# Kernel optimization log

Hardware: AMD Instinct MI355X
Metric: run time of the kernel (lower is better)

Reference implementation:

```python
import jax, jax.numpy as jnp
import numpy as np

N_NODES = 50000
N_EDGES = 800000
IN_DIM = 128
HID = 32
HEADS = 4
OUT_DIM = 128
NEG_SLOPE = 0.2


def setup_inputs() -> dict:
    key = jax.random.key(0)
    ks = jax.random.split(key, 10)
    s = lambda fan_in: 1.0 / np.sqrt(fan_in)
    return {
        "x": jax.random.normal(ks[0], (N_NODES, IN_DIM), dtype=jnp.float32),
        "edge_index": jax.random.randint(ks[1], (2, N_EDGES), 0, N_NODES, dtype=jnp.int64),
        # encoder GATConv: in=IN_DIM, out=HID, heads=HEADS (concat)
        "W1": jax.random.normal(ks[2], (IN_DIM, HEADS * HID), dtype=jnp.float32) * s(IN_DIM),
        "att_src1": jax.random.normal(ks[3], (HEADS, HID), dtype=jnp.float32) * s(HID),
        "att_dst1": jax.random.normal(ks[4], (HEADS, HID), dtype=jnp.float32) * s(HID),
        "b1": jnp.zeros((HEADS * HID,), dtype=jnp.float32),
        # decoder GATConv: in=HEADS*HID, out=OUT_DIM, heads=1
        "W2": jax.random.normal(ks[5], (HEADS * HID, OUT_DIM), dtype=jnp.float32) * s(HEADS * HID),
        "att_src2": jax.random.normal(ks[6], (1, OUT_DIM), dtype=jnp.float32) * s(OUT_DIM),
        "att_dst2": jax.random.normal(ks[7], (1, OUT_DIM), dtype=jnp.float32) * s(OUT_DIM),
        "b2": jnp.zeros((OUT_DIM,), dtype=jnp.float32),
    }


def _gat_conv(x, src, dst, W, att_src, att_dst, bias, heads, out_ch):
    """PyG-style GATConv (v1), eval mode (dropout off), self-loops already in src/dst."""
    n = x.shape[0]
    h = (x @ W).reshape(n, heads, out_ch)                 # [N,H,C]
    a_src = jnp.einsum("nhc,hc->nh", h, att_src)          # [N,H]
    a_dst = jnp.einsum("nhc,hc->nh", h, att_dst)          # [N,H]
    e = jax.nn.leaky_relu(a_src[src] + a_dst[dst], NEG_SLOPE)  # [E,H]
    # segment softmax over destination neighborhoods
    e_max = jax.ops.segment_max(e, dst, num_segments=n)   # [N,H]
    e_exp = jnp.exp(e - e_max[dst])
    denom = jax.ops.segment_sum(e_exp, dst, num_segments=n)
    alpha = e_exp / (denom[dst] + 1e-16)                  # [E,H]
    msg = h[src] * alpha[:, :, None]                      # [E,H,C]
    out = jax.ops.segment_sum(msg, dst, num_segments=n)   # [N,H,C]
    return out.reshape(n, heads * out_ch) + bias


def reference(x, edge_index, W1, att_src1, att_dst1, b1, W2, att_src2, att_dst2, b2):
    n = x.shape[0]
    loops = jnp.arange(n, dtype=edge_index.dtype)
    src = jnp.concatenate([edge_index[0], loops])
    dst = jnp.concatenate([edge_index[1], loops])
    z = jax.nn.relu(_gat_conv(x, src, dst, W1, att_src1, att_dst1, b1, HEADS, HID))
    x_hat = jax.nn.relu(_gat_conv(z, src, dst, W2, att_src2, att_dst2, b2, 1, OUT_DIM))
    return x_hat
```

## Files before the change

kernel.cpp:

```cpp
#include <hip/hip_runtime.h>
#include <hip/hip_bf16.h>
#include <cstddef>

#define N_NODES 50000
#define N_EDGES_RAW 800000
#define E_TOT (N_EDGES_RAW + N_NODES)
#define DIM 128
#define NEG_SLOPE 0.2f

#define NBUCK 196
#define CHUNK 4096
#define NBLK_E ((E_TOT + CHUNK - 1) / CHUNK)
#define CONV_BLKS 3125
#define GB 782

typedef __attribute__((ext_vector_type(8))) short bf16x8;
typedef __attribute__((ext_vector_type(4))) float f32x4;

__device__ __forceinline__ ushort f2bf(float f) {
  unsigned u = __float_as_uint(f);
  return (ushort)((u + 0x7FFFu + ((u >> 16) & 1u)) >> 16);
}
__device__ __forceinline__ float bf2f_lo(uint u) {
  return __uint_as_float(u << 16);
}
__device__ __forceinline__ float bf2f_hi(uint u) {
  return __uint_as_float(u & 0xFFFF0000u);
}

__device__ __forceinline__ void get_edge(const int* __restrict__ ei, int is64,
                                         int e, int& s, int& d) {
  if (e >= N_EDGES_RAW) { s = e - N_EDGES_RAW; d = s; return; }
  if (is64) {
    s = ei[2 * (size_t)e];
    d = ei[2 * ((size_t)N_EDGES_RAW + (size_t)e)];
  } else {
    s = ei[e];
    d = ei[N_EDGES_RAW + e];
  }
}

__device__ __forceinline__ int detect_inline(const int* __restrict__ ei,
                                             int* sflag) {
  const int t = threadIdx.x;
  if (t < 64) {
    int hi = ei[2 * t + 1];
    unsigned long long b = __ballot(hi != 0);
    if (t == 0) *sflag = (b == 0ULL) ? 1 : 0;
  }
  __syncthreads();
  return *sflag;
}

__device__ __forceinline__ void prep_one(const float* __restrict__ w,
                                         const float* __restrict__ atts,
                                         const float* __restrict__ attd,
                                         ushort* __restrict__ wtx,
                                         int H, int idx) {
  const int c = idx >> 7, k = idx & 127;
  const int C = 128 / H;
  float v;
  if (c < 128) {
    v = w[k * 128 + c];
  } else if (c < 128 + H) {
    const int hd = c - 128;
    float s = 0.f;
    for (int j = 0; j < C; ++j) s += w[k * 128 + hd * C + j] * atts[hd * C + j];
    v = s;
  } else if (c < 128 + 2 * H) {
    const int hd = c - 128 - H;
    float s = 0.f;
    for (int j = 0; j < C; ++j) s += w[k * 128 + hd * C + j] * attd[hd * C + j];
    v = s;
  } else {
    v = 0.f;
  }
  wtx[idx] = f2bf(v);
}

__global__ __launch_bounds__(256) void mega_setup(
    const int* __restrict__ ei, int* __restrict__ hist_mat,
    unsigned* __restrict__ pairs,
    const float* __restrict__ W1, const float* __restrict__ as1,
    const float* __restrict__ ad1,
    const float* __restrict__ W2, const float* __restrict__ as2,
    const float* __restrict__ ad2,
    const float* __restrict__ x, ushort* __restrict__ x_bf,
    ushort* __restrict__ wtx1, ushort* __restrict__ wtx2,
    float* __restrict__ w_as2, float* __restrict__ w_ad2) {
  const int b = blockIdx.x, t = threadIdx.x;
  if (b < 72) {
    prep_one(W1, as1, ad1, wtx1, 4, b * 256 + t);
  } else if (b < 136) {
    const int idx = (b - 72) * 256 + t;
    const int c = idx >> 7, k = idx & 127;
    wtx2[idx] = f2bf(W2[k * 128 + c]);
  } else if (b == 136) {
    if (t < 128) {
      float s2 = 0.f, d2 = 0.f;
      for (int c = 0; c < 128; ++c) {
        float w = W2[t * 128 + c];
        s2 += w * as2[c];
        d2 += w * ad2[c];
      }
      w_as2[t] = s2;
      w_ad2[t] = d2;
    }
  } else if (b < 137 + CONV_BLKS) {
    const int base = (b - 137) * 2048 + t * 8;
    float4 v0 = *(const float4*)(x + base);
    float4 v1 = *(const float4*)(x + base + 4);
    ushort u[8];
    u[0] = f2bf(v0.x); u[1] = f2bf(v0.y); u[2] = f2bf(v0.z); u[3] = f2bf(v0.w);
    u[4] = f2bf(v1.x); u[5] = f2bf(v1.y); u[6] = f2bf(v1.z); u[7] = f2bf(v1.w);
    *(uint4*)(x_bf + base) = *(const uint4*)u;
  } else {
    __shared__ int hist[NBUCK];
    __shared__ int sflag;
    const int cb = b - 137 - CONV_BLKS;
    if (t < NBUCK) hist[t] = 0;
    const int is64 = detect_inline(ei, &sflag);
    __syncthreads();
    const int e0 = cb * CHUNK;
#pragma unroll
    for (int i = 0; i < CHUNK / 256; ++i) {
      int e = e0 + i * 256 + t;
      if (e < E_TOT) {
        int s, d;
        get_edge(ei, is64, e, s, d);
        pairs[e] = (unsigned)s | ((unsigned)d << 16);
        atomicAdd(&hist[d >> 8], 1);
      }
    }
    __syncthreads();
    if (t < NBUCK) hist_mat[cb * NBUCK + t] = hist[t];
  }
}

__global__ __launch_bounds__(256) void bucket_scatter(
    const unsigned* __restrict__ pairs, const int* __restrict__ hist_mat,
    unsigned* __restrict__ tmp, int* __restrict__ bstart_g) {
  __shared__ int wtot[4];
  __shared__ int sbase[NBUCK];
  __shared__ int shist[NBUCK];
  const int b = blockIdx.x, t = threadIdx.x, lane = t & 63, wid = t >> 6;
  int tot = 0, pre = 0;
  if (t < NBUCK) {
    for (int bb = 0; bb < NBLK_E; ++bb) {
      int v = hist_mat[bb * NBUCK + t];
      pre += (bb < b) ? v : 0;
      tot += v;
    }
    shist[t] = 0;
  }
  int sc = tot;
#pragma unroll
  for (int m = 1; m < 64; m <<= 1) {
    int o = __shfl_up(sc, m, 64);
    if (lane >= m) sc += o;
  }
  if (lane == 63) wtot[wid] = sc;
  __syncthreads();
  int off = 0;
  for (int w = 0; w < wid; ++w) off += wtot[w];
  const int excl = off + sc - tot;
  if (t < NBUCK) sbase[t] = excl + pre;
  if (b == 0) {
    if (t < NBUCK) bstart_g[t] = excl;
    if (t == 255) bstart_g[NBUCK] = off + sc;
  }
  __syncthreads();
  const int e0 = b * CHUNK;
  unsigned pr_[CHUNK / 256];
  int rk[CHUNK / 256];
#pragma unroll
  for (int i = 0; i < CHUNK / 256; ++i) {
    int e = e0 + i * 256 + t;
    if (e < E_TOT) {
      unsigned pr = pairs[e];
      pr_[i] = pr;
      rk[i] = atomicAdd(&shist[pr >> 24], 1);
    }
  }
#pragma unroll
  for (int i = 0; i < CHUNK / 256; ++i) {
    int e = e0 + i * 256 + t;
    if (e < E_TOT) tmp[sbase[pr_[i] >> 24] + rk[i]] = pr_[i];
  }
}

__device__ __forceinline__ void bucket_sort_body(int b,
                                                 const unsigned* __restrict__ tmp,
                                                 const int* __restrict__ bstart,
                                                 unsigned* __restrict__ csr2,
                                                 int* __restrict__ rp,
                                                 int* __restrict__ deg) {
  __shared__ int cnt[256];
  __shared__ int cur[256];
  __shared__ int wtot2[4];
  const int t = threadIdx.x, lane = t & 63, wid = t >> 6;
  const int p0 = bstart[b], p1 = bstart[b + 1];
  cnt[t] = 0;
  __syncthreads();
  for (int j = p0 + t; j < p1; j += 256) {
    unsigned pr = tmp[j];
    atomicAdd(&cnt[(pr >> 16) & 255u], 1);
  }
  __syncthreads();
  int v = cnt[t];
  int sc = v;
#pragma unroll
  for (int m = 1; m < 64; m <<= 1) {
    int o = __shfl_up(sc, m, 64);
    if (lane >= m) sc += o;
  }
  if (lane == 63) wtot2[wid] = sc;
  __syncthreads();
  int off = 0;
  for (int w = 0; w < wid; ++w) off += wtot2[w];
  const int excl = off + sc - v;
  const int node = b * 256 + t;
  if (node < N_NODES) {
    deg[node] = v;
    rp[node] = p0 + excl;
  }
  cur[t] = excl;
  __syncthreads();
  for (int j = p0 + t; j < p1; j += 256) {
    unsigned pr = tmp[j];
    int ld = (int)((pr >> 16) & 255u);
    int r = atomicAdd(&cur[ld], 1);
    csr2[p0 + r] = pr;
  }
}

__device__ __forceinline__ void gemm_att_body4(int blk,
                                               const ushort* __restrict__ in_bf,
                                               const ushort* __restrict__ wtx,
                                               ushort* __restrict__ h_bf,
                                               float* __restrict__ a_src,
                                               float* __restrict__ a_dst) {
  const int wid = threadIdx.x >> 6;
  const int lane = threadIdx.x & 63;
  const int tile = blk * 4 + wid;
  if (tile >= N_NODES / 16) return;
  const int row0 = tile * 16;
  const int rA = lane & 15;
  const int g = lane >> 4;

  f32x4 acc[9];
#pragma unroll
  for (int ct = 0; ct < 9; ++ct) acc[ct] = (f32x4){0.f, 0.f, 0.f, 0.f};

#pragma unroll
  for (int ks = 0; ks < 4; ++ks) {
    const int k0 = ks * 32 + g * 8;
    bf16x8 af = *(const bf16x8*)(in_bf + (size_t)(row0 + rA) * DIM + k0);
#pragma unroll
    for (int ct = 0; ct < 9; ++ct) {
      bf16x8 bf = *(const bf16x8*)(wtx + (size_t)(ct * 16 + rA) * 128 + k0);
      acc[ct] = __builtin_amdgcn_mfma_f32_16x16x32_bf16(af, bf, acc[ct], 0, 0, 0);
    }
  }

#pragma unroll
  for (int ct = 0; ct < 8; ++ct) {
#pragma unroll
    for (int r = 0; r < 4; ++r) {
      const int row = row0 + g * 4 + r;
      h_bf[(size_t)row * DIM + ct * 16 + rA] = f2bf(acc[ct][r]);
    }
  }
  if (rA < 8) {
#pragma unroll
    for (int r = 0; r < 4; ++r) {
      const int row = row0 + g * 4 + r;
      if (rA < 4)
        a_src[(size_t)row * 4 + rA] = acc[8][r];
      else
        a_dst[(size_t)row * 4 + (rA - 4)] = acc[8][r];
    }
  }
}

__global__ __launch_bounds__(256) void gemm4_sort(
    const ushort* __restrict__ x_bf, const ushort* __restrict__ wtx1,
    ushort* __restrict__ h_bf, float* __restrict__ a_src,
    float* __restrict__ a_dst, const unsigned* __restrict__ tmp,
    const int* __restrict__ bstart, unsigned* __restrict__ csr2,
    int* __restrict__ rp, int* __restrict__ deg) {
  if (blockIdx.x < GB)
    gemm_att_body4(blockIdx.x, x_bf, wtx1, h_bf, a_src, a_dst);
  else
    bucket_sort_body(blockIdx.x - GB, tmp, bstart, csr2, rp, deg);
}

__global__ __launch_bounds__(256) void node_agg_l1(
    const int* __restrict__ rp, const int* __restrict__ deg,
    const unsigned* __restrict__ csr2, const ushort* __restrict__ h_bf,
    const float* __restrict__ a_srcv, const float* __restrict__ a_dstv,
    const float* __restrict__ bias, const float* __restrict__ w_as2,
    const float* __restrict__ w_ad2, ushort* __restrict__ z_bf,
    float* __restrict__ a_src2, float* __restrict__ a_dst2) {
  __shared__ float p_lds[4][4][68];
  __shared__ int s_lds[4][64];
  const int wid = threadIdx.x >> 6;
  const int lane = threadIdx.x & 63;
  const int node = blockIdx.x * 4 + wid;
  const int head = lane >> 4;
  const int beg = rp[node];
  const int dg = deg[node];

  float ad[4];
#pragma unroll
  for (int h = 0; h < 4; ++h) ad[h] = a_dstv[(size_t)node * 4 + h];

  float sden = 0.f, ax = 0.f, ay = 0.f;

  for (int c0 = 0; c0 < dg; c0 += 64) {
    const int cnt = min(64, dg - c0);
    if (lane < cnt) {
      int s = (int)(csr2[beg + c0 + lane] & 0xFFFFu);
      s_lds[wid][lane] = s;
      float4 as4 = ((const float4*)a_srcv)[s];
      float vv[4] = {as4.x, as4.y, as4.z, as4.w};
#pragma unroll
      for (int h = 0; h < 4; ++h) {
        float v = vv[h] + ad[h];
        v = v > 0.f ? v : NEG_SLOPE * v;
        v = fminf(fmaxf(v, -60.f), 80.f);
        p_lds[wid][h][lane] = __expf(v);
      }
    }
    int j = 0;
    for (; j + 8 <= cnt; j += 8) {
#pragma unroll
      for (int u = 0; u < 8; ++u) {
        int s = s_lds[wid][j + u];
        float p = p_lds[wid][head][j + u];
        uint hv = *(const uint*)(h_bf + (size_t)s * DIM + 2 * lane);
        ax += p * bf2f_lo(hv);
        ay += p * bf2f_hi(hv);
        sden += p;
      }
    }
    for (; j < cnt; ++j) {
      int s = s_lds[wid][j];
      float p = p_lds[wid][head][j];
      uint hv = *(const uint*)(h_bf + (size_t)s * DIM + 2 * lane);
      ax += p * bf2f_lo(hv);
      ay += p * bf2f_hi(hv);
      sden += p;
    }
  }

  const float inv = 1.f / sden;
  float2 bv = ((const float2*)bias)[lane];
  float ox = fmaxf(ax * inv + bv.x, 0.f);
  float oy = fmaxf(ay * inv + bv.y, 0.f);
  uint u = (uint)f2bf(ox) | ((uint)f2bf(oy) << 16);
  ((uint*)(z_bf + (size_t)node * DIM))[lane] = u;

  float2 ws = ((const float2*)w_as2)[lane];
  float2 wd = ((const float2*)w_ad2)[lane];
  float ps = ox * ws.x + oy * ws.y;
  float pd = ox * wd.x + oy * wd.y;
#pragma unroll
  for (int m = 1; m < 64; m <<= 1) {
    ps += __shfl_xor(ps, m);
    pd += __shfl_xor(pd, m);
  }
  if (lane == 0) {
    a_src2[node] = ps;
    a_dst2[node] = pd;
  }
}

__global__ __launch_bounds__(256) void node_agg_l2(
    const int* __restrict__ rp, const int* __restrict__ deg,
    const unsigned* __restrict__ csr2, const ushort* __restrict__ z_bf,
    const float* __restrict__ a_src2, const float* __restrict__ a_dst2,
    const ushort* __restrict__ wtx2, const float* __restrict__ bias,
    float* __restrict__ outp) {
  __shared__ float p_lds[4][68];
  __shared__ int s_lds[4][64];
  __shared__ ushort u_lds[16][136];
  const int wid = threadIdx.x >> 6;
  const int lane = threadIdx.x & 63;
  const int node = blockIdx.x * 4 + wid;
  const int beg = rp[node];
  const int dg = deg[node];
  const float ad = a_dst2[node];

  float sden = 0.f, ax = 0.f, ay = 0.f;

  for (int c0 = 0; c0 < dg; c0 += 64) {
    const int cnt = min(64, dg - c0);
    if (lane < cnt) {
      int s = (int)(csr2[beg + c0 + lane] & 0xFFFFu);
      s_lds[wid][lane] = s;
      float v = a_src2[s] + ad;
      v = v > 0.f ? v : NEG_SLOPE * v;
      v = fminf(fmaxf(v, -60.f), 80.f);
      p_lds[wid][lane] = __expf(v);
    }
    int j = 0;
    for (; j + 8 <= cnt; j += 8) {
#pragma unroll
      for (int u = 0; u < 8; ++u) {
        int s = s_lds[wid][j + u];
        float p = p_lds[wid][j + u];
        uint hv = *(const uint*)(z_bf + (size_t)s * DIM + 2 * lane);
        ax += p * bf2f_lo(hv);
        ay += p * bf2f_hi(hv);
        sden += p;
      }
    }
    for (; j < cnt; ++j) {
      int s = s_lds[wid][j];
      float p = p_lds[wid][j];
      uint hv = *(const uint*)(z_bf + (size_t)s * DIM + 2 * lane);
      ax += p * bf2f_lo(hv);
      ay += p * bf2f_hi(hv);
      sden += p;
    }
  }

  const float inv = 1.f / sden;
  uint upk = (uint)f2bf(ax * inv) | ((uint)f2bf(ay * inv) << 16);
  ((uint*)(&u_lds[wid][0]))[lane] = upk;
  __syncthreads();

  const int rA = lane & 15;
  const int g = lane >> 4;
  f32x4 acc0 = {0.f, 0.f, 0.f, 0.f}, acc1 = acc0;
#pragma unroll
  for (int ks = 0; ks < 4; ++ks) {
    const int k0 = ks * 32 + g * 8;
    bf16x8 af = *(const bf16x8*)&u_lds[rA][k0];
    bf16x8 b0 = *(const bf16x8*)(wtx2 + (size_t)(wid * 32 + rA) * 128 + k0);
    bf16x8 b1 = *(const bf16x8*)(wtx2 + (size_t)(wid * 32 + 16 + rA) * 128 + k0);
    acc0 = __builtin_amdgcn_mfma_f32_16x16x32_bf16(af, b0, acc0, 0, 0, 0);
    acc1 = __builtin_amdgcn_mfma_f32_16x16x32_bf16(af, b1, acc1, 0, 0, 0);
  }
  if (g == 0) {
#pragma unroll
    for (int q = 0; q < 2; ++q) {
      const int col = wid * 32 + q * 16 + rA;
      const float bv = bias[col];
      const f32x4 a = q == 0 ? acc0 : acc1;
#pragma unroll
      for (int r = 0; r < 4; ++r) {
        outp[(size_t)(blockIdx.x * 4 + r) * DIM + col] = fmaxf(a[r] + bv, 0.f);
      }
    }
  }
}

extern "C" void kernel_launch(void* const* d_in, const int* in_sizes, int n_in,
                              void* d_out, int out_size, void* d_ws, size_t ws_size,
                              hipStream_t stream) {
  const float* x   = (const float*)d_in[0];
  const int*   ei  = (const int*)d_in[1];
  const float* W1  = (const float*)d_in[2];
  const float* as1 = (const float*)d_in[3];
  const float* ad1 = (const float*)d_in[4];
  const float* b1  = (const float*)d_in[5];
  const float* W2  = (const float*)d_in[6];
  const float* as2 = (const float*)d_in[7];
  const float* ad2 = (const float*)d_in[8];
  const float* b2  = (const float*)d_in[9];
  float* out = (float*)d_out;

  char* ws = (char*)d_ws;
  const size_t F_H = (size_t)N_NODES * DIM;
  ushort*   h_bf    = (ushort*)ws;
  ushort*   z_bf    = h_bf + F_H;
  ushort*   x_bf    = z_bf + F_H;
  float*    a_src1  = (float*)(x_bf + F_H);
  float*    a_dst1  = a_src1 + 200000;
  float*    a_src2  = a_dst1 + 200000;
  float*    a_dst2  = a_src2 + N_NODES;
  int*      deg     = (int*)(a_dst2 + N_NODES);
  int*      rp      = deg + N_NODES;
  unsigned* csr2    = (unsigned*)(rp + N_NODES);
  unsigned* tmp     = csr2 + E_TOT;
  unsigned* pairs   = tmp + E_TOT;
  int*      hist_mat= (int*)(pairs + E_TOT);
  int*      bstart  = hist_mat + NBLK_E * NBUCK;
  ushort*   wtx1    = (ushort*)(bstart + NBUCK + 3);
  ushort*   wtx2    = wtx1 + 144 * 128;
  float*    w_as2   = (float*)(wtx2 + 128 * 128);
  float*    w_ad2   = w_as2 + 128;

  const int MEGA = 137 + CONV_BLKS + NBLK_E;
  const int AGG_B = N_NODES / 4;

  hipLaunchKernelGGL(mega_setup, dim3(MEGA), dim3(256), 0, stream,
                     ei, hist_mat, pairs, W1, as1, ad1, W2, as2, ad2,
                     x, x_bf, wtx1, wtx2, w_as2, w_ad2);
  hipLaunchKernelGGL(bucket_scatter, dim3(NBLK_E), dim3(256), 0, stream,
                     pairs, hist_mat, tmp, bstart);
  hipLaunchKernelGGL(gemm4_sort, dim3(GB + NBUCK), dim3(256), 0, stream,
                     x_bf, wtx1, h_bf, a_src1, a_dst1, tmp, bstart, csr2, rp, deg);
  hipLaunchKernelGGL(node_agg_l1, dim3(AGG_B), dim3(256), 0, stream,
                     rp, deg, csr2, h_bf, a_src1, a_dst1, b1, w_as2, w_ad2,
                     z_bf, a_src2, a_dst2);
  hipLaunchKernelGGL(node_agg_l2, dim3(AGG_B), dim3(256), 0, stream,
                     rp, deg, csr2, z_bf, a_src2, a_dst2, wtx2, b2, out);
}
```

Measured before the change: 176.9 us.

## Move layer-2 projection GEMM before aggregation into separate MFMA kernel

The layer-2 linear transform was previously applied after aggregating z (aggregate-then-project, exploiting linearity), with an in-block MFMA plus a __syncthreads. This change adds a standalone gemm_plain kernel computing h2 = z·W2 for all nodes, reusing the x_bf buffer, and makes node_agg_l2 gather h2 rows and apply bias and ReLU directly. It removes the block-level sync and LDS stage from the aggregation kernel, at the cost of an extra launch and a full N×128 bf16 write and read. It also changes rounding, since the projection now happens before the weighted sum.

Measured after the change: 159.9 us. 9.6% less time.

```diff
diff --git a/kernel.cpp b/kernel.cpp
--- a/kernel.cpp
+++ b/kernel.cpp
@@ -295,6 +295,42 @@
     bucket_sort_body(blockIdx.x - GB, tmp, bstart, csr2, rp, deg);
 }
 
+__global__ __launch_bounds__(256) void gemm_plain(const ushort* __restrict__ in_bf,
+                                                  const ushort* __restrict__ wtx,
+                                                  ushort* __restrict__ h_out) {
+  const int wid = threadIdx.x >> 6;
+  const int lane = threadIdx.x & 63;
+  const int tile = blockIdx.x * 4 + wid;
+  if (tile >= N_NODES / 16) return;
+  const int row0 = tile * 16;
+  const int rA = lane & 15;
+  const int g = lane >> 4;
+
+  f32x4 acc[8];
+#pragma unroll
+  for (int ct = 0; ct < 8; ++ct) acc[ct] = (f32x4){0.f, 0.f, 0.f, 0.f};
+
+#pragma unroll
+  for (int ks = 0; ks < 4; ++ks) {
+    const int k0 = ks * 32 + g * 8;
+    bf16x8 af = *(const bf16x8*)(in_bf + (size_t)(row0 + rA) * DIM + k0);
+#pragma unroll
+    for (int ct = 0; ct < 8; ++ct) {
+      bf16x8 bf = *(const bf16x8*)(wtx + (size_t)(ct * 16 + rA) * 128 + k0);
+      acc[ct] = __builtin_amdgcn_mfma_f32_16x16x32_bf16(af, bf, acc[ct], 0, 0, 0);
+    }
+  }
+
+#pragma unroll
+  for (int ct = 0; ct < 8; ++ct) {
+#pragma unroll
+    for (int r = 0; r < 4; ++r) {
+      const int row = row0 + g * 4 + r;
+      h_out[(size_t)row * DIM + ct * 16 + rA] = f2bf(acc[ct][r]);
+    }
+  }
+}
+
 __global__ __launch_bounds__(256) void node_agg_l1(
     const int* __restrict__ rp, const int* __restrict__ deg,
     const unsigned* __restrict__ csr2, const ushort* __restrict__ h_bf,
@@ -378,13 +414,11 @@
 
 __global__ __launch_bounds__(256) void node_agg_l2(
     const int* __restrict__ rp, const int* __restrict__ deg,
-    const unsigned* __restrict__ csr2, const ushort* __restrict__ z_bf,
+    const unsigned* __restrict__ csr2, const ushort* __restrict__ h2,
     const float* __restrict__ a_src2, const float* __restrict__ a_dst2,
-    const ushort* __restrict__ wtx2, const float* __restrict__ bias,
-    float* __restrict__ outp) {
+    const float* __restrict__ bias, float* __restrict__ outp) {
   __shared__ float p_lds[4][68];
   __shared__ int s_lds[4][64];
-  __shared__ ushort u_lds[16][136];
   const int wid = threadIdx.x >> 6;
   const int lane = threadIdx.x & 63;
   const int node = blockIdx.x * 4 + wid;
@@ -410,7 +444,7 @@
       for (int u = 0; u < 8; ++u) {
         int s = s_lds[wid][j + u];
         float p = p_lds[wid][j + u];
-        uint hv = *(const uint*)(z_bf + (size_t)s * DIM + 2 * lane);
+        uint hv = *(const uint*)(h2 + (size_t)s * DIM + 2 * lane);
         ax += p * bf2f_lo(hv);
         ay += p * bf2f_hi(hv);
         sden += p;
@@ -419,7 +453,7 @@
     for (; j < cnt; ++j) {
       int s = s_lds[wid][j];
       float p = p_lds[wid][j];
-      uint hv = *(const uint*)(z_bf + (size_t)s * DIM + 2 * lane);
+      uint hv = *(const uint*)(h2 + (size_t)s * DIM + 2 * lane);
       ax += p * bf2f_lo(hv);
       ay += p * bf2f_hi(hv);
       sden += p;
@@ -427,34 +461,10 @@
   }
 
   const float inv = 1.f / sden;
-  uint upk = (uint)f2bf(ax * inv) | ((uint)f2bf(ay * inv) << 16);
-  ((uint*)(&u_lds[wid][0]))[lane] = upk;
-  __syncthreads();
-
-  const int rA = lane & 15;
-  const int g = lane >> 4;
-  f32x4 acc0 = {0.f, 0.f, 0.f, 0.f}, acc1 = acc0;
-#pragma unroll
-  for (int ks = 0; ks < 4; ++ks) {
-    const int k0 = ks * 32 + g * 8;
-    bf16x8 af = *(const bf16x8*)&u_lds[rA][k0];
-    bf16x8 b0 = *(const bf16x8*)(wtx2 + (size_t)(wid * 32 + rA) * 128 + k0);
-    bf16x8 b1 = *(const bf16x8*)(wtx2 + (size_t)(wid * 32 + 16 + rA) * 128 + k0);
-    acc0 = __builtin_amdgcn_mfma_f32_16x16x32_bf16(af, b0, acc0, 0, 0, 0);
-    acc1 = __builtin_amdgcn_mfma_f32_16x16x32_bf16(af, b1, acc1, 0, 0, 0);
-  }
-  if (g == 0) {
-#pragma unroll
-    for (int q = 0; q < 2; ++q) {
-      const int col = wid * 32 + q * 16 + rA;
-      const float bv = bias[col];
-      const f32x4 a = q == 0 ? acc0 : acc1;
-#pragma unroll
-      for (int r = 0; r < 4; ++r) {
-        outp[(size_t)(blockIdx.x * 4 + r) * DIM + col] = fmaxf(a[r] + bv, 0.f);
-      }
-    }
-  }
+  float2 bv = ((const float2*)bias)[lane];
+  float ox = fmaxf(ax * inv + bv.x, 0.f);
+  float oy = fmaxf(ay * inv + bv.y, 0.f);
+  ((float2*)(outp + (size_t)node * DIM))[lane] = make_float2(ox, oy);
 }
 
 extern "C" void kernel_launch(void* const* d_in, const int* in_sizes, int n_in,
@@ -495,6 +505,7 @@
 
   const int MEGA = 137 + CONV_BLKS + NBLK_E;
   const int AGG_B = N_NODES / 4;
+  ushort* h2 = x_bf;
 
   hipLaunchKernelGGL(mega_setup, dim3(MEGA), dim3(256), 0, stream,
                      ei, hist_mat, pairs, W1, as1, ad1, W2, as2, ad2,
@@ -506,6 +517,8 @@
   hipLaunchKernelGGL(node_agg_l1, dim3(AGG_B), dim3(256), 0, stream,
                      rp, deg, csr2, h_bf, a_src1, a_dst1, b1, w_as2, w_ad2,
                      z_bf, a_src2, a_dst2);
+  hipLaunchKernelGGL(gemm_plain, dim3(GB), dim3(256), 0, stream,
+                     z_bf, wtx2, h2);
   hipLaunchKernelGGL(node_agg_l2, dim3(AGG_B), dim3(256), 0, stream,
-                     rp, deg, csr2, z_bf, a_src2, a_dst2, wtx2, b2, out);
-}
+                     rp, deg, csr2, h2, a_src2, a_dst2, b2, out);
+}
```
